# Kernel optimization log

Measured on AMD Instinct MI355X. Metric: run time of the kernel, lower is better.

The kernel has to match this reference:

```python
import jax, jax.numpy as jnp
import numpy as np

N_NODES = 50000
N_EDGES = 800000
HEADS = 4
OUT_CH = 32
IN_CH = 128
EPS_LN = 1e-5
NEG_SLOPE = 0.2


def setup_inputs() -> dict:
    key = jax.random.key(0)
    ks = jax.random.split(key, 6)
    x = jax.random.normal(ks[0], (N_NODES, IN_CH), dtype=jnp.float32)
    edge_index = jax.random.randint(ks[1], (2, N_EDGES), 0, N_NODES, dtype=jnp.int64)
    # PyG GATConv lin weight (glorot-ish scale), attention vectors, bias, LN params
    W = jax.random.normal(ks[2], (IN_CH, HEADS * OUT_CH), dtype=jnp.float32) / np.sqrt(IN_CH)
    att_src = jax.random.normal(ks[3], (HEADS, OUT_CH), dtype=jnp.float32) / np.sqrt(OUT_CH)
    att_dst = jax.random.normal(ks[4], (HEADS, OUT_CH), dtype=jnp.float32) / np.sqrt(OUT_CH)
    bias = jnp.zeros((HEADS * OUT_CH,), dtype=jnp.float32)
    gamma = jnp.ones((HEADS * OUT_CH,), dtype=jnp.float32)
    beta = jnp.zeros((HEADS * OUT_CH,), dtype=jnp.float32)
    return {"x": x, "edge_index": edge_index, "W": W, "att_src": att_src,
            "att_dst": att_dst, "bias": bias, "gamma": gamma, "beta": beta}


def reference(x, edge_index, W, att_src, att_dst, bias, gamma, beta):
    N = x.shape[0]
    # --- GATConv (concat=True, add_self_loops=True, dropout disabled) ---
    h = (x @ W).reshape(N, HEADS, OUT_CH)                 # [N, H, C]
    a_src = jnp.einsum("nhc,hc->nh", h, att_src)          # [N, H]
    a_dst = jnp.einsum("nhc,hc->nh", h, att_dst)          # [N, H]
    loop = jnp.arange(N, dtype=edge_index.dtype)
    src = jnp.concatenate([edge_index[0], loop])          # [E+N]
    dst = jnp.concatenate([edge_index[1], loop])          # [E+N]
    e = jax.nn.leaky_relu(a_src[src] + a_dst[dst], NEG_SLOPE)  # [E+N, H]
    # segment softmax over incoming edges of each dst node (stable)
    m = jax.ops.segment_max(e, dst, num_segments=N)       # [N, H]
    e = jnp.exp(e - m[dst])
    denom = jax.ops.segment_sum(e, dst, num_segments=N)   # [N, H]
    alpha = e / (denom[dst] + 1e-16)                      # [E+N, H]
    msg = alpha[:, :, None] * h[src]                      # [E+N, H, C]
    out = jax.ops.segment_sum(msg, dst, num_segments=N)   # [N, H, C]
    out = out.reshape(N, HEADS * OUT_CH) + bias
    # --- ELU, (dropout=identity), residual (in==out_dim), LayerNorm ---
    out = jax.nn.elu(out) + x
    mu = out.mean(-1, keepdims=True)
    var = out.var(-1, keepdims=True)
    out = (out - mu) * jax.lax.rsqrt(var + EPS_LN) * gamma + beta
    return out
```

## Files before the change

kernel.cpp:

```cpp
#include <hip/hip_runtime.h>
#include <hip/hip_bf16.h>

constexpr int N_NODES = 50000;
constexpr int N_EDGES = 800000;
constexpr int EN      = N_EDGES + N_NODES;
constexpr int HEADS   = 4;
constexpr int OUT_CH  = 32;
constexpr int HC      = HEADS * OUT_CH;
constexpr float NEG_SLOPE = 0.2f;
constexpr float EPS_LN    = 1e-5f;

constexpr int SCAN_BLK = 1024;
constexpr int SCAN_NB  = (N_NODES + SCAN_BLK - 1) / SCAN_BLK;

__global__ __launch_bounds__(256)
void gemm_att(const float* __restrict__ x, const float* __restrict__ W,
              const float* __restrict__ att_s, const float* __restrict__ att_d,
              float* __restrict__ h, float* __restrict__ asrc, float* __restrict__ adst)
{
    const int t    = threadIdx.x;
    const int c    = t >> 1;
    const int kg   = t & 1;
    const int lane = t & 63;
    const int wv   = t >> 6;

    float Wr[64];
    #pragma unroll
    for (int j = 0; j < 64; ++j)
        Wr[j] = W[(kg * 64 + j) * HC + c];

    const float as = att_s[c];
    const float ad = att_d[c];

    for (int row0 = blockIdx.x * 4; row0 < N_NODES; row0 += gridDim.x * 4) {
        float acc[4] = {0.f, 0.f, 0.f, 0.f};
        #pragma unroll
        for (int r = 0; r < 4; ++r) {
            const float4* xr = (const float4*)(x + (size_t)(row0 + r) * HC + kg * 64);
            #pragma unroll
            for (int j = 0; j < 16; ++j) {
                const float4 xv = xr[j];
                acc[r] += Wr[4*j+0] * xv.x + Wr[4*j+1] * xv.y
                        + Wr[4*j+2] * xv.z + Wr[4*j+3] * xv.w;
            }
        }
        #pragma unroll
        for (int r = 0; r < 4; ++r) {
            const float accf = acc[r] + __shfl_xor(acc[r], 1, 64);
            if (kg == 0) h[(size_t)(row0 + r) * HC + c] = accf;
            float vs = accf * as;
            float vd = accf * ad;
            #pragma unroll
            for (int mb = 2; mb <= 32; mb <<= 1) {
                vs += __shfl_xor(vs, mb, 64);
                vd += __shfl_xor(vd, mb, 64);
            }
            if (lane == 0) {
                asrc[(row0 + r) * HEADS + wv] = vs;
                adst[(row0 + r) * HEADS + wv] = vd;
            }
        }
    }
}

__global__ __launch_bounds__(256)
void deg_hist(const int* __restrict__ ei, unsigned* __restrict__ deg) {
    const int e = blockIdx.x * 256 + threadIdx.x;
    if (e >= EN) return;
    const int dst = (e < N_EDGES) ? ei[N_EDGES + e] : (e - N_EDGES);
    atomicAdd(&deg[dst], 1u);
}

__global__ __launch_bounds__(SCAN_BLK)
void scan_part(const unsigned* __restrict__ deg, unsigned* __restrict__ rs,
               unsigned* __restrict__ bsum)
{
    __shared__ unsigned wsum[16];
    const int tid = threadIdx.x, lane = tid & 63, w = tid >> 6;
    const int i = blockIdx.x * SCAN_BLK + tid;
    const unsigned v = (i < N_NODES) ? deg[i] : 0u;
    unsigned incl = v;
    #pragma unroll
    for (int off = 1; off < 64; off <<= 1) {
        const unsigned nb = __shfl_up(incl, off, 64);
        if (lane >= off) incl += nb;
    }
    if (lane == 63) wsum[w] = incl;
    __syncthreads();
    unsigned woff = 0, total = 0;
    #pragma unroll
    for (int j = 0; j < 16; ++j) {
        const unsigned tv = wsum[j];
        if (j < w) woff += tv;
        total += tv;
    }
    if (i < N_NODES) rs[i] = woff + incl - v;
    if (tid == 0) bsum[blockIdx.x] = total;
}

__global__ __launch_bounds__(64)
void scan_tops(unsigned* __restrict__ bsum)
{
    const int lane = threadIdx.x;
    const unsigned v = (lane < SCAN_NB) ? bsum[lane] : 0u;
    unsigned incl = v;
    #pragma unroll
    for (int off = 1; off < 64; off <<= 1) {
        const unsigned nb = __shfl_up(incl, off, 64);
        if (lane >= off) incl += nb;
    }
    if (lane < SCAN_NB) bsum[lane] = incl - v;
}

__global__ __launch_bounds__(SCAN_BLK)
void scan_add(const unsigned* __restrict__ bsum, unsigned* __restrict__ rs)
{
    const int i = blockIdx.x * SCAN_BLK + threadIdx.x;
    if (i < N_NODES) rs[i] += bsum[blockIdx.x];
    if (i == 0) rs[N_NODES] = (unsigned)EN;
}

__global__ __launch_bounds__(256)
void scatter_edges(const int* __restrict__ ei, const unsigned* __restrict__ rs,
                   unsigned* __restrict__ cursor, int* __restrict__ esrc) {
    const int e = blockIdx.x * 256 + threadIdx.x;
    if (e >= EN) return;
    const int src = (e < N_EDGES) ? ei[e] : (e - N_EDGES);
    const int dst = (e < N_EDGES) ? ei[N_EDGES + e] : (e - N_EDGES);
    const unsigned pos = rs[dst] + atomicAdd(&cursor[dst], 1u);
    esrc[pos] = src;
}

__global__ __launch_bounds__(256)
void gat_aggregate(const int* __restrict__ esrc, const unsigned* __restrict__ rs,
                   const float* __restrict__ asrc, const float* __restrict__ adst,
                   const float* __restrict__ h, const float* __restrict__ x,
                   const float* __restrict__ bias, const float* __restrict__ gamma,
                   const float* __restrict__ beta, float* __restrict__ out)
{
    const int wv   = threadIdx.x >> 6;
    const int lane = threadIdx.x & 63;
    const int n    = blockIdx.x * 4 + wv;
    const int hh   = lane >> 4;
    const int start = (int)rs[n], end = (int)rs[n + 1];
    const float adn = adst[n * HEADS + hh];

    float m = -INFINITY, s = 0.f, ax = 0.f, ay = 0.f;
    int pos = start;
    for (; pos + 1 < end; pos += 2) {
        const int s0 = esrc[pos], s1 = esrc[pos + 1];
        float v0 = asrc[s0 * HEADS + hh] + adn;
        float v1 = asrc[s1 * HEADS + hh] + adn;
        v0 = (v0 > 0.f) ? v0 : NEG_SLOPE * v0;
        v1 = (v1 > 0.f) ? v1 : NEG_SLOPE * v1;
        const float2 h0 = ((const float2*)(h + (size_t)s0 * HC))[lane];
        const float2 h1 = ((const float2*)(h + (size_t)s1 * HC))[lane];
        const float nm = fmaxf(m, fmaxf(v0, v1));
        const float cs = expf(m - nm);
        const float w0 = expf(v0 - nm);
        const float w1 = expf(v1 - nm);
        ax = ax * cs + w0 * h0.x + w1 * h1.x;
        ay = ay * cs + w0 * h0.y + w1 * h1.y;
        s  = s  * cs + w0 + w1;
        m = nm;
    }
    if (pos < end) {
        const int s0 = esrc[pos];
        float v0 = asrc[s0 * HEADS + hh] + adn;
        v0 = (v0 > 0.f) ? v0 : NEG_SLOPE * v0;
        const float2 h0 = ((const float2*)(h + (size_t)s0 * HC))[lane];
        const float nm = fmaxf(m, v0);
        const float cs = expf(m - nm);
        const float w0 = expf(v0 - nm);
        ax = ax * cs + w0 * h0.x;
        ay = ay * cs + w0 * h0.y;
        s  = s  * cs + w0;
    }

    const float inv = 1.f / (s + 1e-16f);
    const float2 bv = ((const float2*)bias)[lane];
    const float2 xv = ((const float2*)(x + (size_t)n * HC))[lane];
    float ox = ax * inv + bv.x;
    float oy = ay * inv + bv.y;
    ox = (ox > 0.f) ? ox : expm1f(ox);
    oy = (oy > 0.f) ? oy : expm1f(oy);
    ox += xv.x; oy += xv.y;

    float ss = ox + oy, sq = ox * ox + oy * oy;
    #pragma unroll
    for (int off = 32; off >= 1; off >>= 1) {
        ss += __shfl_xor(ss, off, 64);
        sq += __shfl_xor(sq, off, 64);
    }
    const float mu   = ss * (1.f / HC);
    const float var  = sq * (1.f / HC) - mu * mu;
    const float rstd = rsqrtf(var + EPS_LN);
    const float2 gv = ((const float2*)gamma)[lane];
    const float2 bt = ((const float2*)beta)[lane];
    float2 ov;
    ov.x = (ox - mu) * rstd * gv.x + bt.x;
    ov.y = (oy - mu) * rstd * gv.y + bt.y;
    ((float2*)(out + (size_t)n * HC))[lane] = ov;
}

extern "C" void kernel_launch(void* const* d_in, const int* in_sizes, int n_in,
                              void* d_out, int out_size, void* d_ws, size_t ws_size,
                              hipStream_t stream) {
    const float* x     = (const float*)d_in[0];
    const int*   ei    = (const int*)  d_in[1];
    const float* W     = (const float*)d_in[2];
    const float* att_s = (const float*)d_in[3];
    const float* att_d = (const float*)d_in[4];
    const float* bias  = (const float*)d_in[5];
    const float* gamma = (const float*)d_in[6];
    const float* beta  = (const float*)d_in[7];
    float* out = (float*)d_out;

    char* ws = (char*)d_ws;
    float*    h      = (float*)   (ws);
    float*    asrc   = (float*)   (ws + 25600000);
    float*    adst   = (float*)   (ws + 26400000);
    unsigned* deg    = (unsigned*)(ws + 27200000);
    unsigned* cursor = (unsigned*)(ws + 27400000);
    unsigned* rs     = (unsigned*)(ws + 27600000);
    unsigned* bsum   = (unsigned*)(ws + 27800192);
    int*      esrc   = (int*)     (ws + 27800448);

    hipMemsetAsync(deg,    0, (size_t)N_NODES * 4, stream);
    hipMemsetAsync(cursor, 0, (size_t)N_NODES * 4, stream);

    gemm_att<<<1024, 256, 0, stream>>>(x, W, att_s, att_d, h, asrc, adst);

    const int e_grid = (EN + 255) / 256;
    deg_hist     <<<e_grid, 256, 0, stream>>>(ei, deg);
    scan_part    <<<SCAN_NB, SCAN_BLK, 0, stream>>>(deg, rs, bsum);
    scan_tops    <<<1, 64, 0, stream>>>(bsum);
    scan_add     <<<SCAN_NB, SCAN_BLK, 0, stream>>>(bsum, rs);
    scatter_edges<<<e_grid, 256, 0, stream>>>(ei, rs, cursor, esrc);

    gat_aggregate<<<N_NODES / 4, 256, 0, stream>>>(esrc, rs, asrc, adst, h, x,
                                                   bias, gamma, beta, out);
}
```

Measured before the change: 476.2 us.

## Stage x rows in shared memory and compute two output columns per thread in GEMM

The GEMM+attention kernel now uses 128-thread blocks, each thread holding two W column slices (128 registers of weights) and computing columns cc and cc+64. Eight x rows are staged cooperatively into LDS per iteration instead of every thread reading them from global memory, and the attention reductions are restructured with half-weighting so the pair-sum is folded into the butterfly. This raises arithmetic reuse per x load but greatly increases register pressure, which may reduce occupancy or cause spills.

```diff
diff --git a/kernel.cpp b/kernel.cpp
--- a/kernel.cpp
+++ b/kernel.cpp
@@ -13,51 +13,74 @@
 constexpr int SCAN_BLK = 1024;
 constexpr int SCAN_NB  = (N_NODES + SCAN_BLK - 1) / SCAN_BLK;
 
-__global__ __launch_bounds__(256)
+__global__ __launch_bounds__(128)
 void gemm_att(const float* __restrict__ x, const float* __restrict__ W,
               const float* __restrict__ att_s, const float* __restrict__ att_d,
               float* __restrict__ h, float* __restrict__ asrc, float* __restrict__ adst)
 {
+    __shared__ float xs[8 * HC];
     const int t    = threadIdx.x;
-    const int c    = t >> 1;
+    const int cc   = t >> 1;
     const int kg   = t & 1;
     const int lane = t & 63;
     const int wv   = t >> 6;
 
-    float Wr[64];
-    #pragma unroll
-    for (int j = 0; j < 64; ++j)
-        Wr[j] = W[(kg * 64 + j) * HC + c];
-
-    const float as = att_s[c];
-    const float ad = att_d[c];
-
-    for (int row0 = blockIdx.x * 4; row0 < N_NODES; row0 += gridDim.x * 4) {
-        float acc[4] = {0.f, 0.f, 0.f, 0.f};
+    float Wlo[64], Whi[64];
+    #pragma unroll
+    for (int j = 0; j < 64; ++j) {
+        Wlo[j] = W[(kg * 64 + j) * HC + cc];
+        Whi[j] = W[(kg * 64 + j) * HC + cc + 64];
+    }
+    const float as_lo = att_s[cc],      ad_lo = att_d[cc];
+    const float as_hi = att_s[cc + 64], ad_hi = att_d[cc + 64];
+
+    const float4* xsv = (const float4*)xs;
+
+    for (int row0 = blockIdx.x * 8; row0 < N_NODES; row0 += gridDim.x * 8) {
+        __syncthreads();
+        ((float4*)xs)[t]       = ((const float4*)(x + (size_t)row0 * HC))[t];
+        ((float4*)xs)[t + 128] = ((const float4*)(x + (size_t)row0 * HC))[t + 128];
+        __syncthreads();
+
+        float alo[8], ahi[8];
         #pragma unroll
-        for (int r = 0; r < 4; ++r) {
-            const float4* xr = (const float4*)(x + (size_t)(row0 + r) * HC + kg * 64);
+        for (int r = 0; r < 8; ++r) { alo[r] = 0.f; ahi[r] = 0.f; }
+
+        #pragma unroll
+        for (int r = 0; r < 8; ++r) {
             #pragma unroll
             for (int j = 0; j < 16; ++j) {
-                const float4 xv = xr[j];
-                acc[r] += Wr[4*j+0] * xv.x + Wr[4*j+1] * xv.y
-                        + Wr[4*j+2] * xv.z + Wr[4*j+3] * xv.w;
+                const float4 xv = xsv[r * 32 + kg * 16 + j];
+                alo[r] += Wlo[4*j+0] * xv.x + Wlo[4*j+1] * xv.y
+                        + Wlo[4*j+2] * xv.z + Wlo[4*j+3] * xv.w;
+                ahi[r] += Whi[4*j+0] * xv.x + Whi[4*j+1] * xv.y
+                        + Whi[4*j+2] * xv.z + Whi[4*j+3] * xv.w;
             }
         }
+
         #pragma unroll
-        for (int r = 0; r < 4; ++r) {
-            const float accf = acc[r] + __shfl_xor(acc[r], 1, 64);
-            if (kg == 0) h[(size_t)(row0 + r) * HC + c] = accf;
-            float vs = accf * as;
-            float vd = accf * ad;
+        for (int r = 0; r < 8; ++r) {
+            const int row = row0 + r;
+            const float flo = alo[r] + __shfl_xor(alo[r], 1, 64);
+            const float fhi = ahi[r] + __shfl_xor(ahi[r], 1, 64);
+            if (kg == 0) h[(size_t)row * HC + cc]      = flo;
+            else         h[(size_t)row * HC + cc + 64] = fhi;
+            float vs = 0.5f * (flo * as_lo);
+            float vd = 0.5f * (flo * ad_lo);
+            float ws_ = 0.5f * (fhi * as_hi);
+            float wd = 0.5f * (fhi * ad_hi);
             #pragma unroll
-            for (int mb = 2; mb <= 32; mb <<= 1) {
+            for (int mb = 1; mb <= 32; mb <<= 1) {
                 vs += __shfl_xor(vs, mb, 64);
                 vd += __shfl_xor(vd, mb, 64);
+                ws_ += __shfl_xor(ws_, mb, 64);
+                wd += __shfl_xor(wd, mb, 64);
             }
             if (lane == 0) {
-                asrc[(row0 + r) * HEADS + wv] = vs;
-                adst[(row0 + r) * HEADS + wv] = vd;
+                asrc[row * HEADS + wv]     = vs;
+                adst[row * HEADS + wv]     = vd;
+                asrc[row * HEADS + wv + 2] = ws_;
+                adst[row * HEADS + wv + 2] = wd;
             }
         }
     }
@@ -229,7 +252,7 @@
     hipMemsetAsync(deg,    0, (size_t)N_NODES * 4, stream);
     hipMemsetAsync(cursor, 0, (size_t)N_NODES * 4, stream);
 
-    gemm_att<<<1024, 256, 0, stream>>>(x, W, att_s, att_d, h, asrc, adst);
+    gemm_att<<<1536, 128, 0, stream>>>(x, W, att_s, att_d, h, asrc, adst);
 
     const int e_grid = (EN + 255) / 256;
     deg_hist     <<<e_grid, 256, 0, stream>>>(ei, deg);
```

After: 423.9 us. 11.0% less time.
